# Kernel optimization log

Hardware: AMD Instinct MI355X
Metric: run time of the kernel (lower is better)

The kernel has to match this reference:

```python
import jax, jax.numpy as jnp
import numpy as np

A, B, C, D, DT, STEPS = 0.02, 0.2, -65.0, 8.0, 1.0, 100
H, I, O = 8192, 4096, 4096


def _compress(x, gain):
    return jnp.sign(x) * jnp.log1p(gain * jnp.abs(x) + 1e-6)


def setup_inputs() -> dict:
    key = jax.random.key(0)
    k1, k2, k3, k4, k5 = jax.random.split(key, 5)
    return {
        "v_input": jax.random.normal(k1, (I,), jnp.float32),
        "target_output": jax.random.normal(k2, (O,), jnp.float32),
        "W1": jax.random.uniform(k3, (H, I), jnp.float32) * 0.05,
        "W2": jax.random.uniform(k4, (O, H), jnp.float32) * 0.05,
        "W_feedback": jax.random.uniform(k5, (H, O), jnp.float32) * 0.02,
        "gain1": jnp.float32(1.0),
        "gain2": jnp.float32(1.0),
    }


def reference(v_input, target_output, W1, W2, W_feedback, gain1, gain2):
    # Input currents are loop-invariant in the original torch loop; compute once.
    I_hidden = _compress(W1 @ v_input, gain1)            # [H]
    I_output = _compress(W2 @ I_hidden, gain2)           # [O]
    I_hidden = I_hidden - W_feedback @ I_output          # [H]
    total_input = jnp.concatenate([I_hidden, I_output])  # [H+O]

    n = total_input.shape[0]
    v0 = jnp.full((n,), -65.0, jnp.float32)
    u0 = B * v0

    def step(carry, _):
        v_prev, u_prev = carry
        v = v_prev + DT * (0.04 * v_prev ** 2 + 5.0 * v_prev + 0.14 - u_prev + total_input)
        u = u_prev + DT * A * (B * v_prev - u_prev)
        spiked = v >= 30.0
        v = jnp.where(spiked, C, v)
        u = jnp.where(spiked, u + D, u)
        return (v, u), (v, u)

    _, (vs, us) = jax.lax.scan(step, (v0, u0), None, length=STEPS - 1)
    v_vec = jnp.concatenate([v0[None, :], vs], axis=0)  # [STEPS, H+O]
    u_vec = jnp.concatenate([u0[None, :], us], axis=0)

    loss = jnp.mean((I_output - target_output) ** 2)
    return loss, v_vec, u_vec
```

## Files before the change

kernel.cpp:

```cpp
#include <hip/hip_runtime.h>
#include <math.h>

#define HSZ 8192
#define ISZ 4096
#define OSZ 4096
#define NTOT (HSZ + OSZ)
#define STEPS 100

__device__ __forceinline__ float bf2f(unsigned short h) {
    union { unsigned u; float f; } c; c.u = ((unsigned)h) << 16; return c.f;
}

__device__ __forceinline__ double compress_d(double x, double gain) {
    double s = (x > 0.0) ? 1.0 : ((x < 0.0) ? -1.0 : 0.0);
    return s * log1p(gain * fabs(x) + 1e-6);
}

__device__ __forceinline__ double wred(double a) {
    #pragma unroll
    for (int o = 32; o > 0; o >>= 1) a += __shfl_down(a, o, 64);
    return a;
}

__global__ void detect_kernel(const void* W1, int* flag) {
    if (threadIdx.x == 0 && blockIdx.x == 0) {
        const unsigned short* p = (const unsigned short*)W1;
        int bf = 1;
        for (int i = 0; i < 128; ++i) {
            unsigned short a = (unsigned short)(p[i] & 0x7FFF);
            if (a > 0x3D80) bf = 0;
        }
        *flag = bf;
    }
}

template <int C, int XIN>
__global__ void mv_compress(const void* __restrict__ W, const void* __restrict__ x,
                            const void* __restrict__ gain, float* __restrict__ y,
                            const int* __restrict__ flag) {
    const int wave = threadIdx.x >> 6, lane = threadIdx.x & 63;
    const int row = blockIdx.x * 4 + wave;
    const int bf = *flag;
    double acc = 0.0;
    if (bf) {
        const ushort4* Wr = (const ushort4*)((const unsigned short*)W + (size_t)row * C);
        if (XIN) {
            const ushort4* xv = (const ushort4*)x;
            for (int it = 0; it < C / 256; ++it) {
                const int i = it * 64 + lane;
                ushort4 w = Wr[i], xx = xv[i];
                acc += (double)bf2f(w.x) * (double)bf2f(xx.x);
                acc += (double)bf2f(w.y) * (double)bf2f(xx.y);
                acc += (double)bf2f(w.z) * (double)bf2f(xx.z);
                acc += (double)bf2f(w.w) * (double)bf2f(xx.w);
            }
        } else {
            const float4* xv = (const float4*)x;
            for (int it = 0; it < C / 256; ++it) {
                const int i = it * 64 + lane;
                ushort4 w = Wr[i]; float4 xx = xv[i];
                acc += (double)bf2f(w.x) * (double)xx.x;
                acc += (double)bf2f(w.y) * (double)xx.y;
                acc += (double)bf2f(w.z) * (double)xx.z;
                acc += (double)bf2f(w.w) * (double)xx.w;
            }
        }
    } else {
        const float4* Wr = (const float4*)((const float*)W + (size_t)row * C);
        const float4* xv = (const float4*)x;
        for (int it = 0; it < C / 256; ++it) {
            const int i = it * 64 + lane;
            float4 w = Wr[i], xx = xv[i];
            acc += (double)w.x * (double)xx.x;
            acc += (double)w.y * (double)xx.y;
            acc += (double)w.z * (double)xx.z;
            acc += (double)w.w * (double)xx.w;
        }
    }
    acc = wred(acc);
    if (lane == 0) {
        float g = bf ? bf2f(*(const unsigned short*)gain) : *(const float*)gain;
        y[row] = (float)compress_d(acc, (double)g);
    }
}

__global__ void mv_feedback(const void* __restrict__ Wfb, const float* __restrict__ io,
                            const float* __restrict__ h1c, float* __restrict__ hid,
                            const int* __restrict__ flag) {
    const int wave = threadIdx.x >> 6, lane = threadIdx.x & 63;
    const int row = blockIdx.x * 4 + wave;
    const int bf = *flag;
    double acc = 0.0;
    const float4* xv = (const float4*)io;
    if (bf) {
        const ushort4* Wr = (const ushort4*)((const unsigned short*)Wfb + (size_t)row * OSZ);
        for (int it = 0; it < OSZ / 256; ++it) {
            const int i = it * 64 + lane;
            ushort4 w = Wr[i]; float4 xx = xv[i];
            acc += (double)bf2f(w.x) * (double)xx.x;
            acc += (double)bf2f(w.y) * (double)xx.y;
            acc += (double)bf2f(w.z) * (double)xx.z;
            acc += (double)bf2f(w.w) * (double)xx.w;
        }
    } else {
        const float4* Wr = (const float4*)((const float*)Wfb + (size_t)row * OSZ);
        for (int it = 0; it < OSZ / 256; ++it) {
            const int i = it * 64 + lane;
            float4 w = Wr[i], xx = xv[i];
            acc += (double)w.x * (double)xx.x;
            acc += (double)w.y * (double)xx.y;
            acc += (double)w.z * (double)xx.z;
            acc += (double)w.w * (double)xx.w;
        }
    }
    acc = wred(acc);
    if (lane == 0) hid[row] = h1c[row] - (float)acc;
}

__global__ void loss_kernel(const float* __restrict__ io, const void* __restrict__ tgt,
                            float* __restrict__ out, const int* __restrict__ flag) {
    __shared__ double red[4];
    const int bf = *flag;
    double acc = 0.0;
    for (int i = threadIdx.x; i < OSZ; i += 256) {
        float t = bf ? bf2f(((const unsigned short*)tgt)[i]) : ((const float*)tgt)[i];
        double d = (double)io[i] - (double)t;
        acc += d * d;
    }
    acc = wred(acc);
    if ((threadIdx.x & 63) == 0) red[threadIdx.x >> 6] = acc;
    __syncthreads();
    if (threadIdx.x == 0)
        out[0] = (float)((red[0] + red[1] + red[2] + red[3]) / (double)OSZ);
}

__global__ void sim_kernel(const float* __restrict__ hid, const float* __restrict__ io,
                           float* __restrict__ vout, float* __restrict__ uout) {
    const int n = blockIdx.x * blockDim.x + threadIdx.x;
    if (n >= NTOT) return;
    const float ti = (n < HSZ) ? hid[n] : io[n - HSZ];
    float v = -65.0f;
    float u = 0.2f * v;
    vout[n] = v;
    uout[n] = u;
    for (int s = 1; s < STEPS; ++s) {
        float dv = 0.04f * (v * v);
        dv = dv + 5.0f * v;
        dv = dv + 0.14f;
        dv = dv - u;
        dv = dv + ti;
        float vn = v + 1.0f * dv;
        float du = 0.2f * v - u;
        float un = u + 0.02f * du;
        bool sp = (vn >= 30.0f);
        v = sp ? -65.0f : vn;
        u = sp ? (un + 8.0f) : un;
        vout[(size_t)s * NTOT + n] = v;
        uout[(size_t)s * NTOT + n] = u;
    }
}

extern "C" void kernel_launch(void* const* d_in, const int* in_sizes, int n_in,
                              void* d_out, int out_size, void* d_ws, size_t ws_size,
                              hipStream_t stream) {
    const void* v_input = d_in[0];
    const void* target  = d_in[1];
    const void* W1      = d_in[2];
    const void* W2      = d_in[3];
    const void* Wfb     = d_in[4];
    const void* gain1   = d_in[5];
    const void* gain2   = d_in[6];

    float* out  = (float*)d_out;
    float* vout = out + 1;
    float* uout = out + 1 + (size_t)STEPS * NTOT;

    int*   flag = (int*)d_ws;
    float* base = (float*)((char*)d_ws + 256);
    float* h1c  = base;
    float* io   = base + HSZ;
    float* hid  = io + OSZ;

    detect_kernel<<<1, 64, 0, stream>>>(W1, flag);
    mv_compress<ISZ, 1><<<HSZ / 4, 256, 0, stream>>>(W1, v_input, gain1, h1c, flag);
    mv_compress<HSZ, 0><<<OSZ / 4, 256, 0, stream>>>(W2, h1c, gain2, io, flag);
    mv_feedback<<<HSZ / 4, 256, 0, stream>>>(Wfb, io, h1c, hid, flag);
    loss_kernel<<<1, 256, 0, stream>>>(io, target, out, flag);
    sim_kernel<<<NTOT / 256, 256, 0, stream>>>(hid, io, vout, uout);
}
```

Before: 380.5 us.

## Fuse dtype detection into kernels, merge loss with simulation, widen bf16 loads

Drops the separate detect kernel: each wave now checks the dtype inline with a ballot over the first 128 W1 values. The loss reduction is merged into the simulation launch as an extra block, and the simulation now uses 64-thread blocks. The matvec kernels are unified into one template that loads 8 bf16 weights per 16-byte access and fully unrolls the loop. This cuts launch count and per-kernel overhead. It adds a redundant detection read in every wave, and the small sim blocks may hurt occupancy.

```diff
diff --git a/kernel.cpp b/kernel.cpp
--- a/kernel.cpp
+++ b/kernel.cpp
@@ -6,9 +6,16 @@
 #define OSZ 4096
 #define NTOT (HSZ + OSZ)
 #define STEPS 100
+#define SIMB (NTOT / 64)
 
 __device__ __forceinline__ float bf2f(unsigned short h) {
     union { unsigned u; float f; } c; c.u = ((unsigned)h) << 16; return c.f;
+}
+
+__device__ __forceinline__ float2 upk(unsigned u) {
+    union { unsigned q; float f; } lo, hi;
+    lo.q = u << 16; hi.q = u & 0xffff0000u;
+    float2 r; r.x = lo.f; r.y = hi.f; return r;
 }
 
 __device__ __forceinline__ double compress_d(double x, double gain) {
@@ -22,125 +29,96 @@
     return a;
 }
 
-__global__ void detect_kernel(const void* W1, int* flag) {
-    if (threadIdx.x == 0 && blockIdx.x == 0) {
-        const unsigned short* p = (const unsigned short*)W1;
-        int bf = 1;
-        for (int i = 0; i < 128; ++i) {
-            unsigned short a = (unsigned short)(p[i] & 0x7FFF);
-            if (a > 0x3D80) bf = 0;
-        }
-        *flag = bf;
-    }
+__device__ __forceinline__ int detect_bf16(const void* W1) {
+    const unsigned short* p = (const unsigned short*)W1;
+    const int lane = threadIdx.x & 63;
+    unsigned short a0 = (unsigned short)(p[lane] & 0x7FFF);
+    unsigned short a1 = (unsigned short)(p[lane + 64] & 0x7FFF);
+    unsigned long long bad = __ballot((a0 > 0x3D80) || (a1 > 0x3D80));
+    return bad == 0ull;
 }
 
-template <int C, int XIN>
-__global__ void mv_compress(const void* __restrict__ W, const void* __restrict__ x,
-                            const void* __restrict__ gain, float* __restrict__ y,
-                            const int* __restrict__ flag) {
+template <int C, int XIN, int FB>
+__global__ __launch_bounds__(256) void mv_kernel(const void* __restrict__ W,
+                                                 const void* __restrict__ x,
+                                                 const void* __restrict__ gain,
+                                                 const float* __restrict__ prev,
+                                                 float* __restrict__ y,
+                                                 const void* __restrict__ W1ref) {
     const int wave = threadIdx.x >> 6, lane = threadIdx.x & 63;
-    const int row = blockIdx.x * 4 + wave;
-    const int bf = *flag;
+    const int row  = blockIdx.x * 4 + wave;
+    const int bf   = detect_bf16(W1ref);
     double acc = 0.0;
     if (bf) {
-        const ushort4* Wr = (const ushort4*)((const unsigned short*)W + (size_t)row * C);
-        if (XIN) {
-            const ushort4* xv = (const ushort4*)x;
-            for (int it = 0; it < C / 256; ++it) {
-                const int i = it * 64 + lane;
-                ushort4 w = Wr[i], xx = xv[i];
-                acc += (double)bf2f(w.x) * (double)bf2f(xx.x);
-                acc += (double)bf2f(w.y) * (double)bf2f(xx.y);
-                acc += (double)bf2f(w.z) * (double)bf2f(xx.z);
-                acc += (double)bf2f(w.w) * (double)bf2f(xx.w);
+        const uint4* Wr = (const uint4*)((const unsigned short*)W + (size_t)row * C);
+        #pragma unroll
+        for (int it = 0; it < C / 512; ++it) {
+            const int i = it * 64 + lane;
+            uint4 w = Wr[i];
+            float2 w0 = upk(w.x), w1 = upk(w.y), w2 = upk(w.z), w3 = upk(w.w);
+            float x0, x1, x2, x3, x4, x5, x6, x7;
+            if (XIN) {
+                uint4 xx = ((const uint4*)x)[i];
+                float2 p0 = upk(xx.x), p1 = upk(xx.y), p2 = upk(xx.z), p3 = upk(xx.w);
+                x0 = p0.x; x1 = p0.y; x2 = p1.x; x3 = p1.y;
+                x4 = p2.x; x5 = p2.y; x6 = p3.x; x7 = p3.y;
+            } else {
+                const float4* xv = (const float4*)x;
+                float4 xa = xv[i * 2], xb = xv[i * 2 + 1];
+                x0 = xa.x; x1 = xa.y; x2 = xa.z; x3 = xa.w;
+                x4 = xb.x; x5 = xb.y; x6 = xb.z; x7 = xb.w;
             }
-        } else {
-            const float4* xv = (const float4*)x;
-            for (int it = 0; it < C / 256; ++it) {
-                const int i = it * 64 + lane;
-                ushort4 w = Wr[i]; float4 xx = xv[i];
-                acc += (double)bf2f(w.x) * (double)xx.x;
-                acc += (double)bf2f(w.y) * (double)xx.y;
-                acc += (double)bf2f(w.z) * (double)xx.z;
-                acc += (double)bf2f(w.w) * (double)xx.w;
-            }
+            acc += (double)w0.x * x0 + (double)w0.y * x1;
+            acc += (double)w1.x * x2 + (double)w1.y * x3;
+            acc += (double)w2.x * x4 + (double)w2.y * x5;
+            acc += (double)w3.x * x6 + (double)w3.y * x7;
         }
     } else {
         const float4* Wr = (const float4*)((const float*)W + (size_t)row * C);
         const float4* xv = (const float4*)x;
+        #pragma unroll
         for (int it = 0; it < C / 256; ++it) {
             const int i = it * 64 + lane;
             float4 w = Wr[i], xx = xv[i];
-            acc += (double)w.x * (double)xx.x;
-            acc += (double)w.y * (double)xx.y;
-            acc += (double)w.z * (double)xx.z;
-            acc += (double)w.w * (double)xx.w;
+            acc += (double)w.x * (double)xx.x + (double)w.y * (double)xx.y;
+            acc += (double)w.z * (double)xx.z + (double)w.w * (double)xx.w;
         }
     }
     acc = wred(acc);
     if (lane == 0) {
-        float g = bf ? bf2f(*(const unsigned short*)gain) : *(const float*)gain;
-        y[row] = (float)compress_d(acc, (double)g);
+        if (FB) {
+            y[row] = prev[row] - (float)acc;
+        } else {
+            float g = bf ? bf2f(*(const unsigned short*)gain) : *(const float*)gain;
+            y[row] = (float)compress_d(acc, (double)g);
+        }
     }
 }
 
-__global__ void mv_feedback(const void* __restrict__ Wfb, const float* __restrict__ io,
-                            const float* __restrict__ h1c, float* __restrict__ hid,
-                            const int* __restrict__ flag) {
-    const int wave = threadIdx.x >> 6, lane = threadIdx.x & 63;
-    const int row = blockIdx.x * 4 + wave;
-    const int bf = *flag;
-    double acc = 0.0;
-    const float4* xv = (const float4*)io;
-    if (bf) {
-        const ushort4* Wr = (const ushort4*)((const unsigned short*)Wfb + (size_t)row * OSZ);
-        for (int it = 0; it < OSZ / 256; ++it) {
-            const int i = it * 64 + lane;
-            ushort4 w = Wr[i]; float4 xx = xv[i];
-            acc += (double)bf2f(w.x) * (double)xx.x;
-            acc += (double)bf2f(w.y) * (double)xx.y;
-            acc += (double)bf2f(w.z) * (double)xx.z;
-            acc += (double)bf2f(w.w) * (double)xx.w;
+__global__ __launch_bounds__(64) void sim_loss_kernel(const float* __restrict__ hid,
+                                                      const float* __restrict__ io,
+                                                      const void* __restrict__ tgt,
+                                                      const void* __restrict__ W1ref,
+                                                      float* __restrict__ out) {
+    float* vout = out + 1;
+    float* uout = out + 1 + (size_t)STEPS * NTOT;
+    if (blockIdx.x == SIMB) {
+        const int lane = threadIdx.x;
+        const int bf = detect_bf16(W1ref);
+        double acc = 0.0;
+        for (int i = lane; i < OSZ; i += 64) {
+            float t = bf ? bf2f(((const unsigned short*)tgt)[i]) : ((const float*)tgt)[i];
+            double d = (double)io[i] - (double)t;
+            acc += d * d;
         }
-    } else {
-        const float4* Wr = (const float4*)((const float*)Wfb + (size_t)row * OSZ);
-        for (int it = 0; it < OSZ / 256; ++it) {
-            const int i = it * 64 + lane;
-            float4 w = Wr[i], xx = xv[i];
-            acc += (double)w.x * (double)xx.x;
-            acc += (double)w.y * (double)xx.y;
-            acc += (double)w.z * (double)xx.z;
-            acc += (double)w.w * (double)xx.w;
-        }
+        acc = wred(acc);
+        if (lane == 0) out[0] = (float)(acc / (double)OSZ);
+        return;
     }
-    acc = wred(acc);
-    if (lane == 0) hid[row] = h1c[row] - (float)acc;
-}
-
-__global__ void loss_kernel(const float* __restrict__ io, const void* __restrict__ tgt,
-                            float* __restrict__ out, const int* __restrict__ flag) {
-    __shared__ double red[4];
-    const int bf = *flag;
-    double acc = 0.0;
-    for (int i = threadIdx.x; i < OSZ; i += 256) {
-        float t = bf ? bf2f(((const unsigned short*)tgt)[i]) : ((const float*)tgt)[i];
-        double d = (double)io[i] - (double)t;
-        acc += d * d;
-    }
-    acc = wred(acc);
-    if ((threadIdx.x & 63) == 0) red[threadIdx.x >> 6] = acc;
-    __syncthreads();
-    if (threadIdx.x == 0)
-        out[0] = (float)((red[0] + red[1] + red[2] + red[3]) / (double)OSZ);
-}
-
-__global__ void sim_kernel(const float* __restrict__ hid, const float* __restrict__ io,
-                           float* __restrict__ vout, float* __restrict__ uout) {
-    const int n = blockIdx.x * blockDim.x + threadIdx.x;
-    if (n >= NTOT) return;
+    const int n = blockIdx.x * 64 + threadIdx.x;
     const float ti = (n < HSZ) ? hid[n] : io[n - HSZ];
     float v = -65.0f;
-    float u = 0.2f * v;
+    float u = -13.0f;
     vout[n] = v;
     uout[n] = u;
     for (int s = 1; s < STEPS; ++s) {
@@ -171,20 +149,14 @@
     const void* gain1   = d_in[5];
     const void* gain2   = d_in[6];
 
-    float* out  = (float*)d_out;
-    float* vout = out + 1;
-    float* uout = out + 1 + (size_t)STEPS * NTOT;
+    float* out = (float*)d_out;
 
-    int*   flag = (int*)d_ws;
-    float* base = (float*)((char*)d_ws + 256);
-    float* h1c  = base;
-    float* io   = base + HSZ;
-    float* hid  = io + OSZ;
+    float* h1c = (float*)d_ws;
+    float* io  = h1c + HSZ;
+    float* hid = io + OSZ;
 
-    detect_kernel<<<1, 64, 0, stream>>>(W1, flag);
-    mv_compress<ISZ, 1><<<HSZ / 4, 256, 0, stream>>>(W1, v_input, gain1, h1c, flag);
-    mv_compress<HSZ, 0><<<OSZ / 4, 256, 0, stream>>>(W2, h1c, gain2, io, flag);
-    mv_feedback<<<HSZ / 4, 256, 0, stream>>>(Wfb, io, h1c, hid, flag);
-    loss_kernel<<<1, 256, 0, stream>>>(io, target, out, flag);
-    sim_kernel<<<NTOT / 256, 256, 0, stream>>>(hid, io, vout, uout);
+    mv_kernel<ISZ, 1, 0><<<HSZ / 4, 256, 0, stream>>>(W1, v_input, gain1, nullptr, h1c, W1);
+    mv_kernel<HSZ, 0, 0><<<OSZ / 4, 256, 0, stream>>>(W2, h1c, gain2, nullptr, io, W1);
+    mv_kernel<OSZ, 0, 1><<<HSZ / 4, 256, 0, stream>>>(Wfb, io, nullptr, h1c, hid, W1);
+    sim_loss_kernel<<<SIMB + 1, 64, 0, stream>>>(hid, io, target, W1, out);
 }
```

Measured after the change: 390.5 us. 2.6% more time.
